# Kernel optimization log

Measured on AMD Instinct MI355X. Metric: run time of the kernel, lower is better.

## Reference

```python
import jax, jax.numpy as jnp
import numpy as np


def setup_inputs() -> dict:
    key = jax.random.key(0)
    k1, k2 = jax.random.split(key)
    B, S = 2048, 512
    # effective pixel intensity samples (positive), per pixel over time
    it_eff = jax.random.uniform(k1, (B, S), minval=0.05, maxval=1.05, dtype=jnp.float32)
    # strictly increasing sample timestamps, dt ~ 1e-4 s
    dts = jax.random.uniform(k2, (B, S), minval=5e-5, maxval=1.5e-4, dtype=jnp.float32)
    ts = jnp.cumsum(dts, axis=1)
    return {
        "it_eff": it_eff,
        "ts": ts,
        # buffer (no softplus): tau_in * it_eff product constant
        "tau_in_it_eff_prod": jnp.float32(1e-4),
        # raw (pre-softplus) learned parameters, softplus(raw) = actual value
        "tau_mil_raw": jnp.float32(-9.0),    # tau_mil_it_eff_prod ~ 1.2e-4
        "A_amp_inv_raw": jnp.float32(-3.0),  # A_amp ~ 20.6
        "A_loop_inv_raw": jnp.float32(-4.0), # A_loop ~ 55
        "tau_out_raw": jnp.float32(-8.0),    # tau_out ~ 3.4e-4 s
        "tau_sf_raw": jnp.float32(-9.0),     # tau_sf ~ 1.2e-4 s
        "tau_diff_raw": jnp.float32(-10.0),  # tau_diff ~ 4.5e-5 s
    }


def _forward(it_eff, ts, tau_in_it_eff_prod, tau_mil_raw, A_amp_inv_raw,
             A_loop_inv_raw, tau_out_raw, tau_sf_raw, tau_diff_raw):
    sp = jax.nn.softplus
    tau_mil_prod = sp(tau_mil_raw)
    A_amp = 1.0 / sp(A_amp_inv_raw)
    A_loop = 1.0 / sp(A_loop_inv_raw)
    tau_out = sp(tau_out_raw)
    omega_c_sf = 1.0 / sp(tau_sf_raw)
    omega_c_diff = 1.0 / sp(tau_diff_raw)

    B, S = it_eff.shape
    K = S - 1
    u = jnp.log(it_eff)                      # effective log-intensity input
    dt = ts[:, 1:] - ts[:, :-1]              # [B, K]

    # Linearize NLTI photoreceptor LPF at steady state = next input sample
    I_ss = it_eff[:, 1:]                     # [B, K]
    tau_in = tau_in_it_eff_prod / I_ss
    tau_mil = tau_mil_prod / I_ss
    denom = (tau_in + tau_mil) * tau_out
    two_zeta_omega_n = (tau_in + tau_out + (A_amp + 1.0) * tau_mil) / denom
    omega_n_sq = (A_loop + 1.0) / denom

    # Augmented matrix for FOH discretization: expm([[A*dt, B*dt, 0],[0,0,1],[0,0,0]])
    # top-left -> Ad, col 4 -> Gamma1, col 5 -> Gamma2 (FOH ramp integral / dt)
    em = jnp.zeros((B, K, 6, 6), dtype=it_eff.dtype)
    em = (em.at[..., 0, 0].set(-two_zeta_omega_n * dt)
            .at[..., 0, 1].set(-omega_n_sq * dt)
            .at[..., 1, 0].set(dt)
            .at[..., 2, 1].set(omega_c_sf * dt)
            .at[..., 2, 2].set(-omega_c_sf * dt)
            .at[..., 3, 2].set(omega_c_diff * dt)
            .at[..., 3, 3].set(-omega_c_diff * dt)
            .at[..., 0, 4].set(omega_n_sq * dt)
            .at[..., 4, 5].set(1.0))
    ms = jax.vmap(jax.scipy.linalg.expm)(em.reshape(-1, 6, 6)).reshape(B, K, 6, 6)
    Ad = ms[..., :4, :4]                     # [B, K, 4, 4]
    G1 = ms[..., :4, 4]                      # [B, K, 4]
    G2 = ms[..., :4, 5]                      # [B, K, 4]
    Bd = G1 - G2                             # coeff of u[k]
    Bt = G2                                  # coeff of u[k+1] (FOH)

    # steady-state initial state at u[0]: x = [0, u0, u0, u0]
    u0 = u[:, 0]
    x0 = jnp.stack([jnp.zeros_like(u0), u0, u0, u0], axis=-1)  # [B, 4]

    def step(x, inp):
        Ad_k, Bd_k, Bt_k, u_k, u_k1 = inp
        x_new = (jnp.einsum('bij,bj->bi', Ad_k, x)
                 + Bd_k * u_k[:, None] + Bt_k * u_k1[:, None])
        return x_new, x_new[:, 3]            # diff-amp LPF output state

    xs = (jnp.moveaxis(Ad, 1, 0), jnp.moveaxis(Bd, 1, 0), jnp.moveaxis(Bt, 1, 0),
          u[:, :-1].T, u[:, 1:].T)
    _, ys = jax.lax.scan(step, x0, xs)       # ys: [K, B]
    y = jnp.concatenate([u0[:, None], ys.T], axis=1)  # [B, S]
    return y


def reference(it_eff, ts, tau_in_it_eff_prod, tau_mil_raw, A_amp_inv_raw,
              A_loop_inv_raw, tau_out_raw, tau_sf_raw, tau_diff_raw):
    return _forward(it_eff, ts, tau_in_it_eff_prod, tau_mil_raw, A_amp_inv_raw,
                    A_loop_inv_raw, tau_out_raw, tau_sf_raw, tau_diff_raw)
```

## Files before the change

kernel.cpp:

```cpp
#include <hip/hip_runtime.h>
#include <math.h>

namespace {
constexpr int BB  = 2048;
constexpr int SS  = 512;
constexpr int TPB = 128;
constexpr int NSQ = 4;
constexpr float SCV = 0.0625f;
}

__device__ __forceinline__ float frcp(float x) { return __builtin_amdgcn_rcpf(x); }
__device__ __forceinline__ float frsq(float x) { return __builtin_amdgcn_rsqf(x); }
__device__ __forceinline__ float flog(float x) {
    return __builtin_amdgcn_logf(x) * 0.69314718056f;
}

struct Aff {
    float a00, a01, a10, a11;
    float a20, a21, a22;
    float a30, a31, a32, a33;
    float c0, c1, c2, c3;
};

__device__ __forceinline__ Aff aff_identity() {
    Aff r;
    r.a00 = 1.f; r.a01 = 0.f; r.a10 = 0.f; r.a11 = 1.f;
    r.a20 = 0.f; r.a21 = 0.f; r.a22 = 1.f;
    r.a30 = 0.f; r.a31 = 0.f; r.a32 = 0.f; r.a33 = 1.f;
    r.c0 = 0.f; r.c1 = 0.f; r.c2 = 0.f; r.c3 = 0.f;
    return r;
}

__device__ __forceinline__ Aff aff_compose(const Aff& s, const Aff& f) {
    Aff r;
    r.a00 = s.a00*f.a00 + s.a01*f.a10;
    r.a01 = s.a00*f.a01 + s.a01*f.a11;
    r.a10 = s.a10*f.a00 + s.a11*f.a10;
    r.a11 = s.a10*f.a01 + s.a11*f.a11;
    r.a20 = s.a20*f.a00 + s.a21*f.a10 + s.a22*f.a20;
    r.a21 = s.a20*f.a01 + s.a21*f.a11 + s.a22*f.a21;
    r.a22 = s.a22*f.a22;
    r.a30 = s.a30*f.a00 + s.a31*f.a10 + s.a32*f.a20 + s.a33*f.a30;
    r.a31 = s.a30*f.a01 + s.a31*f.a11 + s.a32*f.a21 + s.a33*f.a31;
    r.a32 = s.a32*f.a22 + s.a33*f.a32;
    r.a33 = s.a33*f.a33;
    r.c0 = s.a00*f.c0 + s.a01*f.c1 + s.c0;
    r.c1 = s.a10*f.c0 + s.a11*f.c1 + s.c1;
    r.c2 = s.a20*f.c0 + s.a21*f.c1 + s.a22*f.c2 + s.c2;
    r.c3 = s.a30*f.c0 + s.a31*f.c1 + s.a32*f.c2 + s.a33*f.c3 + s.c3;
    return r;
}

__device__ __forceinline__ Aff aff_shfl_up(const Aff& a, int d) {
    Aff r;
    r.a00 = __shfl_up(a.a00, d, 64); r.a01 = __shfl_up(a.a01, d, 64);
    r.a10 = __shfl_up(a.a10, d, 64); r.a11 = __shfl_up(a.a11, d, 64);
    r.a20 = __shfl_up(a.a20, d, 64); r.a21 = __shfl_up(a.a21, d, 64);
    r.a22 = __shfl_up(a.a22, d, 64);
    r.a30 = __shfl_up(a.a30, d, 64); r.a31 = __shfl_up(a.a31, d, 64);
    r.a32 = __shfl_up(a.a32, d, 64); r.a33 = __shfl_up(a.a33, d, 64);
    r.c0 = __shfl_up(a.c0, d, 64); r.c1 = __shfl_up(a.c1, d, 64);
    r.c2 = __shfl_up(a.c2, d, 64); r.c3 = __shfl_up(a.c3, d, 64);
    return r;
}

__device__ __forceinline__ Aff aff_sel_ident(const Aff& p, bool ok) {
    Aff r;
    r.a00 = ok ? p.a00 : 1.f; r.a01 = ok ? p.a01 : 0.f;
    r.a10 = ok ? p.a10 : 0.f; r.a11 = ok ? p.a11 : 1.f;
    r.a20 = ok ? p.a20 : 0.f; r.a21 = ok ? p.a21 : 0.f;
    r.a22 = ok ? p.a22 : 1.f;
    r.a30 = ok ? p.a30 : 0.f; r.a31 = ok ? p.a31 : 0.f;
    r.a32 = ok ? p.a32 : 0.f; r.a33 = ok ? p.a33 : 1.f;
    r.c0 = ok ? p.c0 : 0.f; r.c1 = ok ? p.c1 : 0.f;
    r.c2 = ok ? p.c2 : 0.f; r.c3 = ok ? p.c3 : 0.f;
    return r;
}

__device__ __forceinline__ void aff_apply(const Aff& m, float& x0, float& x1,
                                          float& x2, float& x3) {
    const float y0 = m.a00*x0 + m.a01*x1 + m.c0;
    const float y1 = m.a10*x0 + m.a11*x1 + m.c1;
    const float y2 = m.a20*x0 + m.a21*x1 + m.a22*x2 + m.c2;
    const float y3 = m.a30*x0 + m.a31*x1 + m.a32*x2 + m.a33*x3 + m.c3;
    x0 = y0; x1 = y1; x2 = y2; x3 = y3;
}

__device__ __forceinline__ Aff make_step(
    float Iss, float dt, float uk, float uk1,
    float sprod, float aprod, float tau_out, float Aloop1,
    float wsf, float wdf, float rwsf, float rwdf)
{
    const float rI  = frcp(Iss);
    const float s   = sprod * rI;
    const float idn = frcp(s * tau_out);
    const float a   = fmaf(aprod, rI, tau_out) * idn;
    const float w2  = Aloop1 * idn;
    const float iw  = frsq(w2);
    const float w   = w2 * iw;

    const float dts = dt * SCV;
    const float f00 = -a * dts;
    const float f01 = -w * dts;
    const float f10 =  w * dts;
    const float f21 =  wsf * dts;
    const float f22 = -f21;
    const float f32 =  wdf * dts;
    const float f33 = -f32;

    float t00 = fmaf(f00, 1.0f/6.0f, 1.0f), t01 = f01 * (1.0f/6.0f);
    float t10 = f10 * (1.0f/6.0f),          t11 = 1.0f;
    float c00 = 0.0f, c01 = f21 * (1.0f/6.0f), c10 = 0.0f, c11 = 0.0f;
    float l00 = fmaf(f22, 1.0f/6.0f, 1.0f);
    float l10 = f32 * (1.0f/6.0f);
    float l11 = fmaf(f33, 1.0f/6.0f, 1.0f);
#pragma unroll
    for (int m = 5; m >= 1; --m) {
        const float rm = 1.0f / (float)m;
        const float p00 = f00*t00 + f01*t10;
        const float p01 = f00*t01 + f01*t11;
        const float p10 = f10*t00;
        const float p11 = f10*t01;
        const float q00 = f21*t10 + f22*c00;
        const float q01 = f21*t11 + f22*c01;
        const float q10 = f32*c00 + f33*c10;
        const float q11 = f32*c01 + f33*c11;
        const float m00 = f22*l00;
        const float m10 = f32*l00 + f33*l10;
        const float m11 = f33*l11;
        t00 = fmaf(p00, rm, 1.0f); t01 = p01*rm;
        t10 = p10*rm;              t11 = fmaf(p11, rm, 1.0f);
        c00 = q00*rm; c01 = q01*rm; c10 = q10*rm; c11 = q11*rm;
        l00 = fmaf(m00, rm, 1.0f); l10 = m10*rm; l11 = fmaf(m11, rm, 1.0f);
    }

#pragma unroll
    for (int i = 0; i < NSQ; ++i) {
        const float p00 = t00*t00 + t01*t10;
        const float p01 = t00*t01 + t01*t11;
        const float p10 = t10*t00 + t11*t10;
        const float p11 = t10*t01 + t11*t11;
        const float q00 = c00*t00 + c01*t10 + l00*c00;
        const float q01 = c00*t01 + c01*t11 + l00*c01;
        const float q10 = c10*t00 + c11*t10 + l10*c00 + l11*c10;
        const float q11 = c10*t01 + c11*t11 + l10*c01 + l11*c11;
        const float m00 = l00*l00;
        const float m10 = l10*l00 + l11*l10;
        const float m11 = l11*l11;
        t00 = p00; t01 = p01; t10 = p10; t11 = p11;
        c00 = q00; c01 = q01; c10 = q10; c11 = q11;
        l00 = m00; l10 = m10; l11 = m11;
    }

    const float aw  = a * iw;
    const float rdt = frcp(dt);
    const float rF  = iw * rdt;
    const float rS  = rwsf * rdt;
    const float rD  = rwdf * rdt;
    const float wS  = w * rwsf;
    const float wD  = w * rwdf;
    const float g0u = w * dt;

    const float y0 = t10;
    const float y1 = -fmaf(aw, t10, t00 - 1.0f);
    const float y2 = fmaf(-wS, c00, y1);
    const float y3 = fmaf(-wD, c10, y2);
    const float s0 = y0 - g0u;
    const float z0 = y1 * rF;
    const float z1 = -fmaf(aw, z0, rF * s0);
    const float z2 = fmaf(-y2, rS, z1);
    const float z3 = fmaf(-y3, rD, z2);

    Aff r;
    r.a00 = t00;      r.a01 = w * t01;
    r.a10 = t10 * iw; r.a11 = t11;
    r.a20 = c00 * iw; r.a21 = c01; r.a22 = l00;
    r.a30 = c10 * iw; r.a31 = c11; r.a32 = l10; r.a33 = l11;
    const float G10 = w * y0, G20 = w * z0;
    const float du = uk1 - uk;
    r.c0 = fmaf(G10, uk, G20 * du);
    r.c1 = fmaf(y1,  uk, z1 * du);
    r.c2 = fmaf(y2,  uk, z2 * du);
    r.c3 = fmaf(y3,  uk, z3 * du);
    return r;
}

__global__ __launch_bounds__(TPB) void pbw_kernel(
    const float* __restrict__ it_eff,
    const float* __restrict__ ts,
    const float* __restrict__ p_tin_prod,
    const float* __restrict__ p_tmil_raw,
    const float* __restrict__ p_aamp_raw,
    const float* __restrict__ p_aloop_raw,
    const float* __restrict__ p_tout_raw,
    const float* __restrict__ p_tsf_raw,
    const float* __restrict__ p_tdiff_raw,
    float* __restrict__ out)
{
    __shared__ float swc[15];
    __shared__ float sy[SS + 4];

    const int b = blockIdx.x;
    const int t = threadIdx.x;
    const int lane = t & 63;
    const int wv = t >> 6;

    const float tin_prod  = p_tin_prod[0];
    const float tmil_prod = log1pf(expf(p_tmil_raw[0]));
    const float Aamp1     = 1.0f / log1pf(expf(p_aamp_raw[0])) + 1.0f;
    const float Aloop1    = 1.0f / log1pf(expf(p_aloop_raw[0])) + 1.0f;
    const float tau_out   = log1pf(expf(p_tout_raw[0]));
    const float sp_sf     = log1pf(expf(p_tsf_raw[0]));
    const float sp_df     = log1pf(expf(p_tdiff_raw[0]));
    const float wsf       = 1.0f / sp_sf;
    const float wdf       = 1.0f / sp_df;
    const float sprod = tin_prod + tmil_prod;
    const float aprod = fmaf(Aamp1, tmil_prod, tin_prod);

    const float* rowI = it_eff + (size_t)b * SS;
    const float* rowT = ts     + (size_t)b * SS;

    const int k0 = 4 * t;
    const float4 I4 = *(const float4*)(rowI + k0);
    const float4 T4 = *(const float4*)(rowT + k0);
    const bool last = (t == TPB - 1);
    const float I_4 = last ? 1.0f : rowI[k0 + 4];
    const float T_4 = last ? (T4.w + 1e-4f) : rowT[k0 + 4];

    const float u_0 = flog(I4.x);
    const float u_1 = flog(I4.y);
    const float u_2 = flog(I4.z);
    const float u_3 = flog(I4.w);
    const float u_4 = flog(I_4);
    const float u0  = flog(rowI[0]);

    Aff m0 = make_step(I4.y, T4.y - T4.x, u_0, u_1,
                       sprod, aprod, tau_out, Aloop1, wsf, wdf, sp_sf, sp_df);
    Aff m1 = make_step(I4.z, T4.z - T4.y, u_1, u_2,
                       sprod, aprod, tau_out, Aloop1, wsf, wdf, sp_sf, sp_df);
    Aff m2 = make_step(I4.w, T4.w - T4.z, u_2, u_3,
                       sprod, aprod, tau_out, Aloop1, wsf, wdf, sp_sf, sp_df);
    Aff m3 = make_step(I_4, T_4 - T4.w, u_3, u_4,
                       sprod, aprod, tau_out, Aloop1, wsf, wdf, sp_sf, sp_df);
    if (last) m3 = aff_identity();

    const Aff c01 = aff_compose(m1, m0);
    const Aff c23 = aff_compose(m3, m2);
    Aff cur = aff_compose(c23, c01);

#pragma unroll
    for (int d = 1; d < 64; d <<= 1) {
        Aff p = aff_shfl_up(cur, d);
        p = aff_sel_ident(p, lane >= d);
        cur = aff_compose(cur, p);
    }

    if (wv == 0 && lane == 63) {
        swc[0]=cur.a00; swc[1]=cur.a01; swc[2]=cur.a10; swc[3]=cur.a11;
        swc[4]=cur.a20; swc[5]=cur.a21; swc[6]=cur.a22;
        swc[7]=cur.a30; swc[8]=cur.a31; swc[9]=cur.a32; swc[10]=cur.a33;
        swc[11]=cur.c0; swc[12]=cur.c1; swc[13]=cur.c2; swc[14]=cur.c3;
    }
    __syncthreads();

    float x0 = 0.0f, x1 = u0, x2 = u0, x3 = u0;
    if (wv == 1) {
        Aff wm;
        wm.a00=swc[0]; wm.a01=swc[1]; wm.a10=swc[2]; wm.a11=swc[3];
        wm.a20=swc[4]; wm.a21=swc[5]; wm.a22=swc[6];
        wm.a30=swc[7]; wm.a31=swc[8]; wm.a32=swc[9]; wm.a33=swc[10];
        wm.c0=swc[11]; wm.c1=swc[12]; wm.c2=swc[13]; wm.c3=swc[14];
        aff_apply(wm, x0, x1, x2, x3);
    }

    Aff ex = aff_shfl_up(cur, 1);
    ex = aff_sel_ident(ex, lane >= 1);
    aff_apply(ex, x0, x1, x2, x3);

    aff_apply(m0, x0, x1, x2, x3); sy[k0 + 1] = x3;
    aff_apply(m1, x0, x1, x2, x3); sy[k0 + 2] = x3;
    aff_apply(m2, x0, x1, x2, x3); sy[k0 + 3] = x3;
    aff_apply(m3, x0, x1, x2, x3); sy[k0 + 4] = x3;
    if (t == 0) sy[0] = u0;

    __syncthreads();

    float4* po = (float4*)(out + (size_t)b * SS);
    po[t] = *(const float4*)&sy[4 * t];
}

extern "C" void kernel_launch(void* const* d_in, const int* in_sizes, int n_in,
                              void* d_out, int out_size, void* d_ws, size_t ws_size,
                              hipStream_t stream) {
    const float* it_eff = (const float*)d_in[0];
    const float* ts     = (const float*)d_in[1];
    const float* p2 = (const float*)d_in[2];
    const float* p3 = (const float*)d_in[3];
    const float* p4 = (const float*)d_in[4];
    const float* p5 = (const float*)d_in[5];
    const float* p6 = (const float*)d_in[6];
    const float* p7 = (const float*)d_in[7];
    const float* p8 = (const float*)d_in[8];
    float* out = (float*)d_out;

    pbw_kernel<<<dim3(BB), dim3(TPB), 0, stream>>>(
        it_eff, ts, p2, p3, p4, p5, p6, p7, p8, out);
}
```

Baseline: 91.60 us.

## Split 4-state affine scan into oscillator scan then lower-triangular cascade scan

The block-triangular structure of the state matrix lets the single 15-element affine prefix scan become two smaller scans. The first covers the 2x2 oscillator (6 elements), and the second covers the 2-state lower-triangular filter (5 elements), with the oscillator outputs folded into its offsets. This cuts the shuffle count and FMA work per scan step, which together dominate the wave-level scan. In exchange it adds a second serialized scan pass and an extra __syncthreads, and lengthens the dependency chain.

Measured after the change: 90.68 us. No clear change (-1.0%).

```diff
diff --git a/kernel.cpp b/kernel.cpp
--- a/kernel.cpp
+++ b/kernel.cpp
@@ -31,59 +31,67 @@
     return r;
 }
 
-__device__ __forceinline__ Aff aff_compose(const Aff& s, const Aff& f) {
-    Aff r;
+struct Osc { float a00, a01, a10, a11, c0, c1; };
+
+__device__ __forceinline__ Osc osc_compose(const Osc& s, const Osc& f) {
+    Osc r;
     r.a00 = s.a00*f.a00 + s.a01*f.a10;
     r.a01 = s.a00*f.a01 + s.a01*f.a11;
     r.a10 = s.a10*f.a00 + s.a11*f.a10;
     r.a11 = s.a10*f.a01 + s.a11*f.a11;
-    r.a20 = s.a20*f.a00 + s.a21*f.a10 + s.a22*f.a20;
-    r.a21 = s.a20*f.a01 + s.a21*f.a11 + s.a22*f.a21;
-    r.a22 = s.a22*f.a22;
-    r.a30 = s.a30*f.a00 + s.a31*f.a10 + s.a32*f.a20 + s.a33*f.a30;
-    r.a31 = s.a30*f.a01 + s.a31*f.a11 + s.a32*f.a21 + s.a33*f.a31;
-    r.a32 = s.a32*f.a22 + s.a33*f.a32;
-    r.a33 = s.a33*f.a33;
-    r.c0 = s.a00*f.c0 + s.a01*f.c1 + s.c0;
-    r.c1 = s.a10*f.c0 + s.a11*f.c1 + s.c1;
-    r.c2 = s.a20*f.c0 + s.a21*f.c1 + s.a22*f.c2 + s.c2;
-    r.c3 = s.a30*f.c0 + s.a31*f.c1 + s.a32*f.c2 + s.a33*f.c3 + s.c3;
-    return r;
-}
-
-__device__ __forceinline__ Aff aff_shfl_up(const Aff& a, int d) {
-    Aff r;
+    r.c0  = s.a00*f.c0 + s.a01*f.c1 + s.c0;
+    r.c1  = s.a10*f.c0 + s.a11*f.c1 + s.c1;
+    return r;
+}
+__device__ __forceinline__ Osc osc_shfl_up(const Osc& a, int d) {
+    Osc r;
     r.a00 = __shfl_up(a.a00, d, 64); r.a01 = __shfl_up(a.a01, d, 64);
     r.a10 = __shfl_up(a.a10, d, 64); r.a11 = __shfl_up(a.a11, d, 64);
-    r.a20 = __shfl_up(a.a20, d, 64); r.a21 = __shfl_up(a.a21, d, 64);
-    r.a22 = __shfl_up(a.a22, d, 64);
-    r.a30 = __shfl_up(a.a30, d, 64); r.a31 = __shfl_up(a.a31, d, 64);
-    r.a32 = __shfl_up(a.a32, d, 64); r.a33 = __shfl_up(a.a33, d, 64);
-    r.c0 = __shfl_up(a.c0, d, 64); r.c1 = __shfl_up(a.c1, d, 64);
-    r.c2 = __shfl_up(a.c2, d, 64); r.c3 = __shfl_up(a.c3, d, 64);
-    return r;
-}
-
-__device__ __forceinline__ Aff aff_sel_ident(const Aff& p, bool ok) {
-    Aff r;
+    r.c0  = __shfl_up(a.c0,  d, 64); r.c1  = __shfl_up(a.c1,  d, 64);
+    return r;
+}
+__device__ __forceinline__ Osc osc_sel(const Osc& p, bool ok) {
+    Osc r;
     r.a00 = ok ? p.a00 : 1.f; r.a01 = ok ? p.a01 : 0.f;
     r.a10 = ok ? p.a10 : 0.f; r.a11 = ok ? p.a11 : 1.f;
-    r.a20 = ok ? p.a20 : 0.f; r.a21 = ok ? p.a21 : 0.f;
-    r.a22 = ok ? p.a22 : 1.f;
-    r.a30 = ok ? p.a30 : 0.f; r.a31 = ok ? p.a31 : 0.f;
-    r.a32 = ok ? p.a32 : 0.f; r.a33 = ok ? p.a33 : 1.f;
-    r.c0 = ok ? p.c0 : 0.f; r.c1 = ok ? p.c1 : 0.f;
-    r.c2 = ok ? p.c2 : 0.f; r.c3 = ok ? p.c3 : 0.f;
-    return r;
-}
-
-__device__ __forceinline__ void aff_apply(const Aff& m, float& x0, float& x1,
-                                          float& x2, float& x3) {
-    const float y0 = m.a00*x0 + m.a01*x1 + m.c0;
-    const float y1 = m.a10*x0 + m.a11*x1 + m.c1;
-    const float y2 = m.a20*x0 + m.a21*x1 + m.a22*x2 + m.c2;
-    const float y3 = m.a30*x0 + m.a31*x1 + m.a32*x2 + m.a33*x3 + m.c3;
-    x0 = y0; x1 = y1; x2 = y2; x3 = y3;
+    r.c0  = ok ? p.c0  : 0.f; r.c1  = ok ? p.c1  : 0.f;
+    return r;
+}
+__device__ __forceinline__ void osc_apply(const Osc& m, float& v0, float& v1) {
+    const float y0 = m.a00*v0 + m.a01*v1 + m.c0;
+    const float y1 = m.a10*v0 + m.a11*v1 + m.c1;
+    v0 = y0; v1 = y1;
+}
+
+struct Low { float l00, l10, l11, c0, c1; };
+
+__device__ __forceinline__ Low low_compose(const Low& s, const Low& f) {
+    Low r;
+    r.l00 = s.l00*f.l00;
+    r.l10 = s.l10*f.l00 + s.l11*f.l10;
+    r.l11 = s.l11*f.l11;
+    r.c0  = fmaf(s.l00, f.c0, s.c0);
+    r.c1  = fmaf(s.l10, f.c0, fmaf(s.l11, f.c1, s.c1));
+    return r;
+}
+__device__ __forceinline__ Low low_shfl_up(const Low& a, int d) {
+    Low r;
+    r.l00 = __shfl_up(a.l00, d, 64); r.l10 = __shfl_up(a.l10, d, 64);
+    r.l11 = __shfl_up(a.l11, d, 64);
+    r.c0  = __shfl_up(a.c0,  d, 64); r.c1  = __shfl_up(a.c1,  d, 64);
+    return r;
+}
+__device__ __forceinline__ Low low_sel(const Low& p, bool ok) {
+    Low r;
+    r.l00 = ok ? p.l00 : 1.f; r.l10 = ok ? p.l10 : 0.f;
+    r.l11 = ok ? p.l11 : 1.f;
+    r.c0  = ok ? p.c0  : 0.f; r.c1  = ok ? p.c1  : 0.f;
+    return r;
+}
+__device__ __forceinline__ void low_apply(const Low& m, float& x2, float& x3) {
+    const float y2 = fmaf(m.l00, x2, m.c0);
+    const float y3 = m.l10*x2 + m.l11*x3 + m.c1;
+    x2 = y2; x3 = y3;
 }
 
 __device__ __forceinline__ Aff make_step(
@@ -197,7 +205,8 @@
     const float* __restrict__ p_tdiff_raw,
     float* __restrict__ out)
 {
-    __shared__ float swc[15];
+    __shared__ float swcA[6];
+    __shared__ float swcB[5];
     __shared__ float sy[SS + 4];
 
     const int b = blockIdx.x;
@@ -244,43 +253,77 @@
                        sprod, aprod, tau_out, Aloop1, wsf, wdf, sp_sf, sp_df);
     if (last) m3 = aff_identity();
 
-    const Aff c01 = aff_compose(m1, m0);
-    const Aff c23 = aff_compose(m3, m2);
-    Aff cur = aff_compose(c23, c01);
-
+    const Osc s0 = {m0.a00, m0.a01, m0.a10, m0.a11, m0.c0, m0.c1};
+    const Osc s1 = {m1.a00, m1.a01, m1.a10, m1.a11, m1.c0, m1.c1};
+    const Osc s2 = {m2.a00, m2.a01, m2.a10, m2.a11, m2.c0, m2.c1};
+    const Osc s3 = {m3.a00, m3.a01, m3.a10, m3.a11, m3.c0, m3.c1};
+
+    Osc oc = osc_compose(osc_compose(s3, s2), osc_compose(s1, s0));
 #pragma unroll
     for (int d = 1; d < 64; d <<= 1) {
-        Aff p = aff_shfl_up(cur, d);
-        p = aff_sel_ident(p, lane >= d);
-        cur = aff_compose(cur, p);
-    }
-
+        Osc p = osc_shfl_up(oc, d);
+        p = osc_sel(p, lane >= d);
+        oc = osc_compose(oc, p);
+    }
     if (wv == 0 && lane == 63) {
-        swc[0]=cur.a00; swc[1]=cur.a01; swc[2]=cur.a10; swc[3]=cur.a11;
-        swc[4]=cur.a20; swc[5]=cur.a21; swc[6]=cur.a22;
-        swc[7]=cur.a30; swc[8]=cur.a31; swc[9]=cur.a32; swc[10]=cur.a33;
-        swc[11]=cur.c0; swc[12]=cur.c1; swc[13]=cur.c2; swc[14]=cur.c3;
+        swcA[0]=oc.a00; swcA[1]=oc.a01; swcA[2]=oc.a10; swcA[3]=oc.a11;
+        swcA[4]=oc.c0;  swcA[5]=oc.c1;
     }
     __syncthreads();
 
-    float x0 = 0.0f, x1 = u0, x2 = u0, x3 = u0;
+    float v0 = 0.0f, v1 = u0;
     if (wv == 1) {
-        Aff wm;
-        wm.a00=swc[0]; wm.a01=swc[1]; wm.a10=swc[2]; wm.a11=swc[3];
-        wm.a20=swc[4]; wm.a21=swc[5]; wm.a22=swc[6];
-        wm.a30=swc[7]; wm.a31=swc[8]; wm.a32=swc[9]; wm.a33=swc[10];
-        wm.c0=swc[11]; wm.c1=swc[12]; wm.c2=swc[13]; wm.c3=swc[14];
-        aff_apply(wm, x0, x1, x2, x3);
-    }
-
-    Aff ex = aff_shfl_up(cur, 1);
-    ex = aff_sel_ident(ex, lane >= 1);
-    aff_apply(ex, x0, x1, x2, x3);
-
-    aff_apply(m0, x0, x1, x2, x3); sy[k0 + 1] = x3;
-    aff_apply(m1, x0, x1, x2, x3); sy[k0 + 2] = x3;
-    aff_apply(m2, x0, x1, x2, x3); sy[k0 + 3] = x3;
-    aff_apply(m3, x0, x1, x2, x3); sy[k0 + 4] = x3;
+        Osc wm = {swcA[0], swcA[1], swcA[2], swcA[3], swcA[4], swcA[5]};
+        osc_apply(wm, v0, v1);
+    }
+    Osc oex = osc_shfl_up(oc, 1);
+    oex = osc_sel(oex, lane >= 1);
+    osc_apply(oex, v0, v1);
+
+    const float va0 = v0, vb0 = v1;
+    osc_apply(s0, v0, v1); const float va1 = v0, vb1 = v1;
+    osc_apply(s1, v0, v1); const float va2 = v0, vb2 = v1;
+    osc_apply(s2, v0, v1); const float va3 = v0, vb3 = v1;
+
+    const Low b0 = {m0.a22, m0.a32, m0.a33,
+                    m0.a20*va0 + m0.a21*vb0 + m0.c2,
+                    m0.a30*va0 + m0.a31*vb0 + m0.c3};
+    const Low b1 = {m1.a22, m1.a32, m1.a33,
+                    m1.a20*va1 + m1.a21*vb1 + m1.c2,
+                    m1.a30*va1 + m1.a31*vb1 + m1.c3};
+    const Low b2 = {m2.a22, m2.a32, m2.a33,
+                    m2.a20*va2 + m2.a21*vb2 + m2.c2,
+                    m2.a30*va2 + m2.a31*vb2 + m2.c3};
+    const Low b3 = {m3.a22, m3.a32, m3.a33,
+                    m3.a20*va3 + m3.a21*vb3 + m3.c2,
+                    m3.a30*va3 + m3.a31*vb3 + m3.c3};
+
+    Low lc = low_compose(low_compose(b3, b2), low_compose(b1, b0));
+#pragma unroll
+    for (int d = 1; d < 64; d <<= 1) {
+        Low p = low_shfl_up(lc, d);
+        p = low_sel(p, lane >= d);
+        lc = low_compose(lc, p);
+    }
+    if (wv == 0 && lane == 63) {
+        swcB[0]=lc.l00; swcB[1]=lc.l10; swcB[2]=lc.l11;
+        swcB[3]=lc.c0;  swcB[4]=lc.c1;
+    }
+    __syncthreads();
+
+    float x2 = u0, x3 = u0;
+    if (wv == 1) {
+        Low wm = {swcB[0], swcB[1], swcB[2], swcB[3], swcB[4]};
+        low_apply(wm, x2, x3);
+    }
+    Low lex = low_shfl_up(lc, 1);
+    lex = low_sel(lex, lane >= 1);
+    low_apply(lex, x2, x3);
+
+    low_apply(b0, x2, x3); sy[k0 + 1] = x3;
+    low_apply(b1, x2, x3); sy[k0 + 2] = x3;
+    low_apply(b2, x2, x3); sy[k0 + 3] = x3;
+    low_apply(b3, x2, x3); sy[k0 + 4] = x3;
     if (t == 0) sy[0] = u0;
 
     __syncthreads();
```
